# Optimization experiments

Hardware: AMD Instinct MI355X
Metric: run time of the kernel (lower is better)

Reference implementation:

```python
import math
import jax, jax.numpy as jnp
import numpy as np

B, C_IN, H, W = 32, 96, 64, 64
OUT = 128
EXC = int(OUT * 0.8)   # 102 excitatory channels
INH = OUT - EXC        # 26 inhibitory channels
K = 5
PAD = 2                # kernel//2 so all stages keep spatial size


def _sm_kernel(kernel_size=5, sigma_e=1.2, sigma_i=1.4):
    c = kernel_size // 2
    xx, yy = np.meshgrid(np.arange(kernel_size), np.arange(kernel_size), indexing='ij')
    xx = xx.astype(np.float32) - c
    yy = yy.astype(np.float32) - c
    ge = np.exp(-(xx ** 2 + yy ** 2) / (2 * sigma_e ** 2))
    gi = np.exp(-(xx ** 2 + yy ** 2) / (2 * sigma_i ** 2))
    dog = ge / (2 * math.pi * sigma_e ** 2) - gi / (2 * math.pi * sigma_i ** 2)
    dog = dog / dog[c, c]
    return jnp.asarray(dog[None, None], dtype=jnp.float32)  # [1,1,K,K]


def setup_inputs() -> dict:
    key = jax.random.key(0)
    k1, k2, k3, k4 = jax.random.split(key, 4)
    wr = 25.0 / math.sqrt(C_IN * K * K)
    x = jax.random.normal(k1, (B, C_IN, H, W), jnp.float32)
    w_ee = wr * jnp.abs(jax.random.normal(k2, (EXC, C_IN, K, K), jnp.float32))
    w_ei = wr * jnp.abs(jax.random.normal(k3, (INH, EXC, K, K), jnp.float32))
    w_ie = -wr * jnp.abs(jax.random.normal(k4, (EXC, INH, K, K), jnp.float32))
    return {"x": x, "w_ee": w_ee, "w_ei": w_ei, "w_ie": w_ie, "sm_kernel": _sm_kernel()}


def _reflect_pad(x, p):
    if p == 0:
        return x
    return jnp.pad(x, ((0, 0), (0, 0), (p, p), (p, p)), mode='reflect')


def _conv(x, w, pad=0, groups=1):
    return jax.lax.conv_general_dilated(
        x, w, window_strides=(1, 1), padding=[(pad, pad), (pad, pad)],
        dimension_numbers=('NCHW', 'OIHW', 'NCHW'), feature_group_count=groups)


def _forward(x, w_ee, w_ei, w_ie, sm_kernel):
    y_e = _conv(_reflect_pad(x, PAD), w_ee)                 # [B,EXC,H,W], act=Identity
    y_i = jax.nn.relu(_conv(_reflect_pad(y_e, PAD), w_ei))  # [B,INH,H,W]
    y_ie = _conv(_reflect_pad(y_i, PAD), w_ie)              # [B,EXC,H,W]
    y = y_e + y_ie
    # depthwise surround-modulation conv (zero padding, as in F.conv2d)
    w_sm = jnp.tile(sm_kernel, (EXC, 1, 1, 1))              # [EXC,1,K,K]
    y = _conv(y, w_sm, pad=K // 2, groups=EXC)
    return y, y_e, y_i


def reference(x, w_ee, w_ei, w_ie, sm_kernel):
    y, y_e, y_i = _forward(x, w_ee, w_ei, w_ie, sm_kernel)

    # --- hard WTA masks (winner channel per (b,h,w) position) ---
    win_e = jnp.argmax(y_e, axis=1)                                        # [B,H,W]
    mask_e = (jnp.arange(EXC)[None, :, None, None] == win_e[:, None]).astype(y_e.dtype)
    y_wta_e = y_e * mask_e
    win_i = jnp.argmax(jnp.abs(y_i), axis=1)
    mask_i = (jnp.arange(INH)[None, :, None, None] == win_i[:, None]).astype(y_i.dtype)
    y_wta_i = y_i * mask_i

    # --- transpose-conv outer-product trick; with same-size feature maps the
    # conv collapses to a 1x1 full correlation over (b,h,w) -> einsum ---
    yx_ee = jnp.einsum('bchw,behw->ec', x, y_wta_e)[:, :, None, None]      # [EXC,C_IN,1,1]
    yx_ei = jnp.einsum('behw,bihw->ie', y_wta_e, y_wta_i)[:, :, None, None]  # [INH,EXC,1,1]
    yx_ie = jnp.einsum('bihw,behw->ei', y_wta_i, y)[:, :, None, None]      # [EXC,INH,1,1]

    yu_e = jnp.sum(y_wta_e, axis=(0, 2, 3))[:, None, None, None]           # [EXC,1,1,1]
    yu_i = jnp.sum(jnp.abs(y_wta_i), axis=(0, 2, 3))[:, None, None, None]  # [INH,1,1,1]

    upd_ee = yx_ee - yu_e * w_ee   # broadcasts to [EXC,C_IN,K,K]
    upd_ei = yx_ei - yu_i * w_ei
    upd_ie = yx_ie - yu_e * w_ie
    upd_ee = upd_ee / (jnp.abs(upd_ee).max() + 1e-8)
    upd_ei = upd_ei / (jnp.abs(upd_ei).max() + 1e-8)
    upd_ie = upd_ie / (jnp.abs(upd_ie).max() + 1e-8)

    return (y, upd_ee, upd_ei, upd_ie)
```

## Files before the change

kernel.cpp:

```cpp
#include <hip/hip_runtime.h>

#define B_    32
#define CIN_  96
#define EXC_  102
#define INH_  26
#define HH    64
#define WW    64
#define HW_   4096
#define NPOS  (B_*HW_)
#define EEPAD 97
#define NPART 512
#define NEE   (EXC_*CIN_ + EXC_)
#define NIE   (EXC_*INH_)
#define N1U   (EXC_*CIN_*25)
#define N2U   (INH_*EXC_*25)
#define N3U   (EXC_*INH_*25)

typedef short bf8 __attribute__((ext_vector_type(8)));
typedef float f32x4 __attribute__((ext_vector_type(4)));

__device__ __forceinline__ int refl(int i) {
    if (i < 0) i = -i;
    if (i > 63) i = 126 - i;
    return i;
}

__device__ __forceinline__ short f2bf(float f) {
    unsigned u = __float_as_uint(f);
    return (short)((u + 0x7fffu + ((u >> 16) & 1u)) >> 16);
}

template<int C, int CPAD>
__global__ __launch_bounds__(256) void pack_nhwc(
    const float* __restrict__ src, short* __restrict__ dst)
{
    const int b = blockIdx.z;
    const int pos = blockIdx.x*64 + (threadIdx.x & 63);
    const int cg0 = threadIdx.x >> 6;
    for (int cg = cg0; cg < CPAD/8; cg += 4) {
        bf8 v;
#pragma unroll
        for (int j = 0; j < 8; ++j) {
            int c = cg*8 + j;
            float f = (c < C) ? src[((size_t)b*C + c)*HW_ + pos] : 0.f;
            v[j] = f2bf(f);
        }
        *(bf8*)(&dst[((size_t)b*HW_ + pos)*CPAD + cg*8]) = v;
    }
}

__global__ __launch_bounds__(256) void pack_w3(
    const float* __restrict__ w_ee, const float* __restrict__ w_ei,
    const float* __restrict__ w_ie, short* __restrict__ dst)
{
    int gi = blockIdx.x*256 + threadIdx.x;
    if (gi >= 460800) return;
    const float* src; int N, C, NPAD, CPAD; int idx;
    if (gi < 268800)      { src = w_ee; N = 102; C = 96;  NPAD = 112; CPAD = 96;  idx = gi; }
    else if (gi < 371200) { src = w_ei; N = 26;  C = 102; NPAD = 32;  CPAD = 128; idx = gi - 268800; }
    else                  { src = w_ie; N = 102; C = 26;  NPAD = 112; CPAD = 32;  idx = gi - 371200; }
    int tap = idx / (NPAD*CPAD);
    int rem = idx - tap*(NPAD*CPAD);
    int n = rem / CPAD, c = rem - n*CPAD;
    float f = (n < N && c < C) ? src[((size_t)n*C + c)*25 + tap] : 0.f;
    dst[gi] = f2bf(f);
}

template<int CPAD, int NPAD, int NT, int COUT, int NCHUNK, bool RELU, bool ADDIN>
__global__ __launch_bounds__(256, 2) void conv_mfma(
    const short* __restrict__ src, const short* __restrict__ wgt,
    const float* __restrict__ addin, float* __restrict__ out)
{
    __shared__ __align__(16) short sA[400*40];
    const int t  = threadIdx.x;
    const int bx = blockIdx.x;
    const int b  = blockIdx.z;
    const int h0 = (bx >> 2) * 16;
    const int w0 = (bx &  3) * 16;
    const int lane = t & 63;
    const int wv = t >> 6;
    const int nh = lane & 15;
    const int q  = lane >> 4;

    int goff[7], loff[7];
#pragma unroll
    for (int s = 0; s < 7; ++s) {
        int i = t + 256*s;
        if (i < 1600) {
            int rec = i >> 2, seg = i & 3;
            int lh = rec / 20, lw = rec - lh*20;
            int gh = refl(h0 - 2 + lh), gw = refl(w0 - 2 + lw);
            goff[s] = (b*HW_ + gh*WW + gw) * CPAD + seg*8;
            loff[s] = rec*40 + seg*8;
        } else { goff[s] = 0; loff[s] = -1; }
    }

    f32x4 acc[4][NT];
#pragma unroll
    for (int mt = 0; mt < 4; ++mt)
#pragma unroll
        for (int nt = 0; nt < NT; ++nt) {
            f32x4 z = {0.f, 0.f, 0.f, 0.f};
            acc[mt][nt] = z;
        }

    int abase[4];
#pragma unroll
    for (int mt = 0; mt < 4; ++mt)
        abase[mt] = ((wv*4 + mt)*20 + nh)*40 + q*8;

    for (int ck = 0; ck < NCHUNK; ++ck) {
        const int c0 = ck*32;
        __syncthreads();
#pragma unroll
        for (int s = 0; s < 7; ++s)
            if (loff[s] >= 0)
                *(bf8*)(&sA[loff[s]]) = *(const bf8*)(&src[goff[s] + c0]);
        __syncthreads();
        const short* wch = wgt + c0 + nh*CPAD + q*8;

        bf8 bfr[2][NT];
        bf8 afr[2][4];
        auto LOADTAP = [&](int buf, int tap_) {
            const int dh_ = tap_ / 5, dw_ = tap_ - 5*dh_;
#pragma unroll
            for (int nt = 0; nt < NT; ++nt)
                bfr[buf][nt] = *(const bf8*)(&wch[(size_t)(tap_*NPAD + nt*16)*CPAD]);
#pragma unroll
            for (int mt = 0; mt < 4; ++mt)
                afr[buf][mt] = *(const bf8*)(&sA[abase[mt] + (dh_*20 + dw_)*40]);
        };

        LOADTAP(0, 0);
#pragma unroll
        for (int tap = 0; tap < 25; ++tap) {
            const int cur = tap & 1;
            if (tap < 24) LOADTAP(cur ^ 1, tap + 1);
#pragma unroll
            for (int mt = 0; mt < 4; ++mt)
#pragma unroll
                for (int nt = 0; nt < NT; ++nt)
                    acc[mt][nt] = __builtin_amdgcn_mfma_f32_16x16x32_bf16(
                        afr[cur][mt], bfr[cur][nt], acc[mt][nt], 0, 0, 0);
        }
    }

#pragma unroll
    for (int mt = 0; mt < 4; ++mt) {
        const int rowi = h0 + wv*4 + mt;
#pragma unroll
        for (int nt = 0; nt < NT; ++nt) {
            const int chn = nt*16 + nh;
            if (chn < COUT) {
                size_t obase = ((size_t)(b*COUT + chn))*HW_ + rowi*WW + w0 + q*4;
#pragma unroll
                for (int r = 0; r < 4; ++r) {
                    float v = acc[mt][nt][r];
                    if (RELU) v = fmaxf(v, 0.f);
                    if (ADDIN) v += addin[obase + r];
                    out[obase + r] = v;
                }
            }
        }
    }
}

__global__ __launch_bounds__(256) void smconv_v2(
    const float* __restrict__ in, const float* __restrict__ sm,
    float* __restrict__ out)
{
    __shared__ __align__(16) float sx[36*36];
    const int tid = threadIdx.x;
    const int tile = blockIdx.x;
    const int e = blockIdx.y;
    const int b = blockIdx.z;
    const int h0 = (tile >> 1) * 32, w0 = (tile & 1) * 32;
    const int r  = tid >> 3;
    const int cg = (tid & 7) * 4;
    const float* inc = in + ((size_t)(b*EXC_ + e))*HW_;
#pragma unroll
    for (int it = 0; it < 6; ++it) {
        int i = tid + it*256;
        if (i < 1296) {
            int lh = i / 36, lw = i - lh*36;
            int gh = h0 - 2 + lh, gw = w0 - 2 + lw;
            float v = 0.f;
            if (gh >= 0 && gh < HH && gw >= 0 && gw < WW) v = inc[gh*WW + gw];
            sx[i] = v;
        }
    }
    __syncthreads();
    float a0 = 0.f, a1 = 0.f, a2 = 0.f, a3 = 0.f;
#pragma unroll
    for (int kh = 0; kh < 5; ++kh) {
        const float4* rowp = (const float4*)(sx + (r + kh)*36 + cg);
        float4 v0 = rowp[0], v1 = rowp[1];
        float xv[8] = {v0.x, v0.y, v0.z, v0.w, v1.x, v1.y, v1.z, v1.w};
#pragma unroll
        for (int kw = 0; kw < 5; ++kw) {
            float wv = sm[kh*5 + kw];
            a0 = fmaf(xv[kw+0], wv, a0);
            a1 = fmaf(xv[kw+1], wv, a1);
            a2 = fmaf(xv[kw+2], wv, a2);
            a3 = fmaf(xv[kw+3], wv, a3);
        }
    }
    size_t oidx = ((size_t)(b*EXC_ + e))*HW_ + (h0 + r)*WW + w0 + cg;
    *(float4*)(out + oidx) = make_float4(a0, a1, a2, a3);
}

__global__ void wta_kernel(const float* __restrict__ in, int* __restrict__ win,
                           float* __restrict__ val, int C, int use_abs)
{
    int p = blockIdx.x*256 + threadIdx.x;
    int b = p >> 12, hw = p & 4095;
    const float* base = in + ((size_t)b*C)*HW_ + hw;
    float bestv = base[0];
    float bestk = use_abs ? fabsf(bestv) : bestv;
    int besti = 0;
    for (int c = 1; c < C; ++c) {
        float v = base[(size_t)c*HW_];
        float key = use_abs ? fabsf(v) : v;
        if (key > bestk) { bestk = key; bestv = v; besti = c; }
    }
    win[p] = besti;
    val[p] = bestv;
}

__global__ __launch_bounds__(256) void scatter_ee_kernel(
    const float* __restrict__ x, const int* __restrict__ win_e,
    const float* __restrict__ val_e, float* __restrict__ parts)
{
    __shared__ float s_yx[EXC_*EEPAD];
    __shared__ float s_yu[EXC_];
    for (int i = threadIdx.x; i < EXC_*EEPAD; i += 256) s_yx[i] = 0.f;
    if (threadIdx.x < EXC_) s_yu[threadIdx.x] = 0.f;
    __syncthreads();
    int p = blockIdx.x * 256 + threadIdx.x;
    int b = p >> 12, hw = p & 4095;
    int wi = win_e[p]; float v = val_e[p];
    atomicAdd(&s_yu[wi], v);
    const float* xb = x + ((size_t)b*CIN_)*HW_ + hw;
    float* row = s_yx + wi*EEPAD;
    for (int c = 0; c < CIN_; ++c)
        atomicAdd(&row[c], v * xb[(size_t)c*HW_]);
    __syncthreads();
    float* dst = parts + (size_t)blockIdx.x * NEE;
    for (int i = threadIdx.x; i < EXC_*CIN_; i += 256) {
        int e = i / CIN_, c = i - e*CIN_;
        dst[i] = s_yx[e*EEPAD + c];
    }
    if (threadIdx.x < EXC_) dst[EXC_*CIN_ + threadIdx.x] = s_yu[threadIdx.x];
}

__global__ __launch_bounds__(256) void scatter_ei_kernel(
    const int* __restrict__ win_e, const float* __restrict__ val_e,
    const int* __restrict__ win_i, const float* __restrict__ val_i,
    float* __restrict__ yx_ei, float* __restrict__ yu_i)
{
    __shared__ float s[INH_*EXC_ + INH_];
    for (int i = threadIdx.x; i < INH_*EXC_ + INH_; i += 256) s[i] = 0.f;
    __syncthreads();
    int p = blockIdx.x * 256 + threadIdx.x;
    int we = win_e[p]; float ve = val_e[p];
    int wi = win_i[p]; float vi = val_i[p];
    atomicAdd(&s[wi*EXC_ + we], ve*vi);
    atomicAdd(&s[INH_*EXC_ + wi], fabsf(vi));
    __syncthreads();
    for (int i = threadIdx.x; i < INH_*EXC_ + INH_; i += 256) {
        float v = s[i];
        if (v != 0.f) {
            if (i < INH_*EXC_) atomicAdd(&yx_ei[i], v);
            else               atomicAdd(&yu_i[i - INH_*EXC_], v);
        }
    }
}

__global__ __launch_bounds__(256) void scatter_ie_kernel(
    const float* __restrict__ y, const int* __restrict__ win_i,
    const float* __restrict__ val_i, float* __restrict__ parts)
{
    __shared__ float s[EXC_*INH_];
    for (int i = threadIdx.x; i < EXC_*INH_; i += 256) s[i] = 0.f;
    __syncthreads();
    int p = blockIdx.x * 256 + threadIdx.x;
    int b = p >> 12, hw = p & 4095;
    int wi = win_i[p]; float v = val_i[p];
    if (v != 0.f) {
        const float* yb = y + ((size_t)b*EXC_)*HW_ + hw;
        for (int e = 0; e < EXC_; ++e)
            atomicAdd(&s[e*INH_ + wi], v * yb[(size_t)e*HW_]);
    }
    __syncthreads();
    float* dst = parts + (size_t)blockIdx.x * NIE;
    for (int i = threadIdx.x; i < EXC_*INH_; i += 256) dst[i] = s[i];
}

__global__ __launch_bounds__(256) void reduce_parts_kernel(
    const float* __restrict__ parts, float* __restrict__ dst, int n)
{
    __shared__ float s[256];
    int i = blockIdx.x*64 + (threadIdx.x & 63);
    int g = threadIdx.x >> 6;
    float a = 0.f;
    if (i < n) {
        for (int j = g*128; j < g*128 + 128; ++j)
            a += parts[(size_t)j*n + i];
    }
    s[threadIdx.x] = a;
    __syncthreads();
    if (threadIdx.x < 64 && i < n)
        dst[i] = s[threadIdx.x] + s[threadIdx.x+64] + s[threadIdx.x+128] + s[threadIdx.x+192];
}

__global__ __launch_bounds__(256) void upd_absmax3(
    const float* __restrict__ yx_ee, const float* __restrict__ yu_e,
    const float* __restrict__ w_ee,
    const float* __restrict__ yx_ei, const float* __restrict__ yu_i,
    const float* __restrict__ w_ei,
    const float* __restrict__ yx_ie, const float* __restrict__ w_ie,
    unsigned int* __restrict__ amax)
{
    float m0 = 0.f, m1 = 0.f, m2 = 0.f;
    for (int idx = blockIdx.x*256 + threadIdx.x; idx < N1U + N2U + N3U;
         idx += gridDim.x*256) {
        if (idx < N1U) {
            int ec = idx / 25; int e = ec / CIN_;
            m0 = fmaxf(m0, fabsf(yx_ee[ec] - yu_e[e]*w_ee[idx]));
        } else if (idx < N1U + N2U) {
            int j = idx - N1U; int ec = j / 25; int e = ec / EXC_;
            m1 = fmaxf(m1, fabsf(yx_ei[ec] - yu_i[e]*w_ei[j]));
        } else {
            int j = idx - N1U - N2U; int ec = j / 25; int e = ec / INH_;
            m2 = fmaxf(m2, fabsf(yx_ie[ec] - yu_e[e]*w_ie[j]));
        }
    }
    __shared__ unsigned int s0, s1, s2;
    if (threadIdx.x == 0) { s0 = 0u; s1 = 0u; s2 = 0u; }
    __syncthreads();
    atomicMax(&s0, __float_as_uint(m0));
    atomicMax(&s1, __float_as_uint(m1));
    atomicMax(&s2, __float_as_uint(m2));
    __syncthreads();
    if (threadIdx.x == 0) {
        atomicMax(&amax[0], s0);
        atomicMax(&amax[1], s1);
        atomicMax(&amax[2], s2);
    }
}

__global__ __launch_bounds__(256) void upd_write3(
    const float* __restrict__ yx_ee, const float* __restrict__ yu_e,
    const float* __restrict__ w_ee,
    const float* __restrict__ yx_ei, const float* __restrict__ yu_i,
    const float* __restrict__ w_ei,
    const float* __restrict__ yx_ie, const float* __restrict__ w_ie,
    const unsigned int* __restrict__ amax,
    float* __restrict__ out_ee, float* __restrict__ out_ei,
    float* __restrict__ out_ie)
{
    int idx = blockIdx.x*256 + threadIdx.x;
    if (idx >= N1U + N2U + N3U) return;
    if (idx < N1U) {
        int ec = idx / 25; int e = ec / CIN_;
        float v = yx_ee[ec] - yu_e[e]*w_ee[idx];
        out_ee[idx] = v / (__uint_as_float(amax[0]) + 1e-8f);
    } else if (idx < N1U + N2U) {
        int j = idx - N1U; int ec = j / 25; int e = ec / EXC_;
        float v = yx_ei[ec] - yu_i[e]*w_ei[j];
        out_ei[j] = v / (__uint_as_float(amax[1]) + 1e-8f);
    } else {
        int j = idx - N1U - N2U; int ec = j / 25; int e = ec / INH_;
        float v = yx_ie[ec] - yu_e[e]*w_ie[j];
        out_ie[j] = v / (__uint_as_float(amax[2]) + 1e-8f);
    }
}

extern "C" void kernel_launch(void* const* d_in, const int* in_sizes, int n_in,
                              void* d_out, int out_size, void* d_ws, size_t ws_size,
                              hipStream_t stream)
{
    const float* x    = (const float*)d_in[0];
    const float* w_ee = (const float*)d_in[1];
    const float* w_ei = (const float*)d_in[2];
    const float* w_ie = (const float*)d_in[3];
    const float* smk  = (const float*)d_in[4];
    float* out = (float*)d_out;

    float* y_e = (float*)d_ws;
    float* y_i = y_e + (size_t)B_*EXC_*HW_;
    short* R   = (short*)(y_i + (size_t)B_*INH_*HW_);
    short* wee = R + (size_t)16777216;
    short* wei = wee + 268800;
    short* wie = wei + 102400;
    int*   win_e = (int*)(wie + 89600);
    float* val_e = (float*)(win_e + NPOS);
    int*   win_i = (int*)(val_e + NPOS);
    float* val_i = (float*)(win_i + NPOS);
    float* yx_ee = val_i + NPOS;
    float* yu_e  = yx_ee + EXC_*CIN_;
    float* yx_ie = yu_e + EXC_;
    float* yx_ei = yx_ie + EXC_*INH_;
    float* yu_i  = yx_ei + INH_*EXC_;
    unsigned int* amax = (unsigned int*)(yu_i + INH_);
    float* parts_ee = (float*)R;
    float* parts_ie = parts_ee + (size_t)NPART*NEE;

    hipMemsetAsync(yx_ei, 0, (size_t)(INH_*EXC_ + INH_ + 3)*sizeof(float), stream);

    pack_w3<<<1800, 256, 0, stream>>>(w_ee, w_ei, w_ie, wee);
    pack_nhwc<CIN_, 96><<<dim3(64, 1, B_), 256, 0, stream>>>(x, R);

    conv_mfma<96, 112, 7, EXC_, 3, false, false>
        <<<dim3(16, 1, B_), 256, 0, stream>>>(R, wee, nullptr, y_e);
    wta_kernel<<<NPOS/256, 256, 0, stream>>>(y_e, win_e, val_e, EXC_, 0);

    pack_nhwc<EXC_, 128><<<dim3(64, 1, B_), 256, 0, stream>>>(y_e, R);
    conv_mfma<128, 32, 2, INH_, 4, true, false>
        <<<dim3(16, 1, B_), 256, 0, stream>>>(R, wei, nullptr, y_i);
    wta_kernel<<<NPOS/256, 256, 0, stream>>>(y_i, win_i, val_i, INH_, 1);

    pack_nhwc<INH_, 32><<<dim3(64, 1, B_), 256, 0, stream>>>(y_i, R);
    conv_mfma<32, 112, 7, EXC_, 1, false, true>
        <<<dim3(16, 1, B_), 256, 0, stream>>>(R, wie, y_e, y_e);

    smconv_v2<<<dim3(4, EXC_, B_), 256, 0, stream>>>(y_e, smk, out);

    scatter_ee_kernel<<<NPART, 256, 0, stream>>>(x, win_e, val_e, parts_ee);
    scatter_ei_kernel<<<NPART, 256, 0, stream>>>(win_e, val_e, win_i, val_i, yx_ei, yu_i);
    scatter_ie_kernel<<<NPART, 256, 0, stream>>>(out, win_i, val_i, parts_ie);
    reduce_parts_kernel<<<(NEE + 63)/64, 256, 0, stream>>>(parts_ee, yx_ee, NEE);
    reduce_parts_kernel<<<(NIE + 63)/64, 256, 0, stream>>>(parts_ie, yx_ie, NIE);

    upd_absmax3<<<480, 256, 0, stream>>>(yx_ee, yu_e, w_ee, yx_ei, yu_i, w_ei,
                                         yx_ie, w_ie, amax);
    float* out_ee = out + (size_t)B_*EXC_*HW_;
    float* out_ei = out_ee + N1U;
    float* out_ie = out_ei + N2U;
    upd_write3<<<(N1U + N2U + N3U + 255)/256, 256, 0, stream>>>(
        yx_ee, yu_e, w_ee, yx_ei, yu_i, w_ei, yx_ie, w_ie, amax,
        out_ee, out_ei, out_ie);
}
```

Baseline: 638.0 us.

## Fuse WTA argmax and bf16 NHWC output into conv epilogues, merge small kernels

Winner-take-all argmax is moved into the conv epilogue using a lane shuffle reduction, which removes the two separate WTA passes over y_e and y_i. The second conv now writes bf16 NHWC output directly, so the fp32 y_i tensor and its repack kernel go away. Weight packing, x packing and the memset are merged into one launch, the two scatters are combined, and the two reductions share one kernel. The tap software prefetch in the MFMA loop is replaced by a simpler per-tap load, which may change how well load latency is hidden. The WTA for y_i drops the abs key, which assumes ReLU makes the values non-negative.

```diff
diff --git a/kernel.cpp b/kernel.cpp
--- a/kernel.cpp
+++ b/kernel.cpp
@@ -30,6 +30,42 @@
     return (short)((u + 0x7fffu + ((u >> 16) & 1u)) >> 16);
 }
 
+__global__ __launch_bounds__(256) void pack_all(
+    const float* __restrict__ w_ee, const float* __restrict__ w_ei,
+    const float* __restrict__ w_ie, const float* __restrict__ x,
+    short* __restrict__ wdst, short* __restrict__ xdst,
+    float* __restrict__ zreg)
+{
+    const int blk = blockIdx.x;
+    if (blk < 1800) {
+        int gi = blk*256 + threadIdx.x;
+        if (gi >= 460800) return;
+        const float* src; int N, C, NPAD, CPAD; int idx;
+        if (gi < 268800)      { src = w_ee; N = 102; C = 96;  NPAD = 112; CPAD = 96;  idx = gi; }
+        else if (gi < 371200) { src = w_ei; N = 26;  C = 102; NPAD = 32;  CPAD = 128; idx = gi - 268800; }
+        else                  { src = w_ie; N = 102; C = 26;  NPAD = 112; CPAD = 32;  idx = gi - 371200; }
+        int tap = idx / (NPAD*CPAD);
+        int rem = idx - tap*(NPAD*CPAD);
+        int n = rem / CPAD, c = rem - n*CPAD;
+        float f = (n < N && c < C) ? src[((size_t)n*C + c)*25 + tap] : 0.f;
+        wdst[gi] = f2bf(f);
+    } else if (blk < 3848) {
+        int bb = blk - 1800;
+        int b = bb >> 6, bx = bb & 63;
+        const int pos = bx*64 + (threadIdx.x & 63);
+        const int cg0 = threadIdx.x >> 6;
+        for (int cg = cg0; cg < 96/8; cg += 4) {
+            bf8 v;
+#pragma unroll
+            for (int j = 0; j < 8; ++j)
+                v[j] = f2bf(x[((size_t)b*CIN_ + cg*8 + j)*HW_ + pos]);
+            *(bf8*)(&xdst[((size_t)b*HW_ + pos)*96 + cg*8]) = v;
+        }
+    } else {
+        for (int i = threadIdx.x; i < INH_*EXC_ + INH_ + 3; i += 256) zreg[i] = 0.f;
+    }
+}
+
 template<int C, int CPAD>
 __global__ __launch_bounds__(256) void pack_nhwc(
     const float* __restrict__ src, short* __restrict__ dst)
@@ -49,27 +85,13 @@
     }
 }
 
-__global__ __launch_bounds__(256) void pack_w3(
-    const float* __restrict__ w_ee, const float* __restrict__ w_ei,
-    const float* __restrict__ w_ie, short* __restrict__ dst)
-{
-    int gi = blockIdx.x*256 + threadIdx.x;
-    if (gi >= 460800) return;
-    const float* src; int N, C, NPAD, CPAD; int idx;
-    if (gi < 268800)      { src = w_ee; N = 102; C = 96;  NPAD = 112; CPAD = 96;  idx = gi; }
-    else if (gi < 371200) { src = w_ei; N = 26;  C = 102; NPAD = 32;  CPAD = 128; idx = gi - 268800; }
-    else                  { src = w_ie; N = 102; C = 26;  NPAD = 112; CPAD = 32;  idx = gi - 371200; }
-    int tap = idx / (NPAD*CPAD);
-    int rem = idx - tap*(NPAD*CPAD);
-    int n = rem / CPAD, c = rem - n*CPAD;
-    float f = (n < N && c < C) ? src[((size_t)n*C + c)*25 + tap] : 0.f;
-    dst[gi] = f2bf(f);
-}
-
-template<int CPAD, int NPAD, int NT, int COUT, int NCHUNK, bool RELU, bool ADDIN>
+template<int CPAD, int NPAD, int NT, int COUT, int NCHUNK,
+         bool RELU, bool ADDIN, bool WFLOAT, int OCPAD, bool WTA>
 __global__ __launch_bounds__(256, 2) void conv_mfma(
     const short* __restrict__ src, const short* __restrict__ wgt,
-    const float* __restrict__ addin, float* __restrict__ out)
+    const float* __restrict__ addin, float* __restrict__ out,
+    short* __restrict__ nhwc_out, int* __restrict__ win,
+    float* __restrict__ val)
 {
     __shared__ __align__(16) short sA[400*40];
     const int t  = threadIdx.x;
@@ -118,30 +140,25 @@
                 *(bf8*)(&sA[loff[s]]) = *(const bf8*)(&src[goff[s] + c0]);
         __syncthreads();
         const short* wch = wgt + c0 + nh*CPAD + q*8;
-
-        bf8 bfr[2][NT];
-        bf8 afr[2][4];
-        auto LOADTAP = [&](int buf, int tap_) {
-            const int dh_ = tap_ / 5, dw_ = tap_ - 5*dh_;
-#pragma unroll
-            for (int nt = 0; nt < NT; ++nt)
-                bfr[buf][nt] = *(const bf8*)(&wch[(size_t)(tap_*NPAD + nt*16)*CPAD]);
-#pragma unroll
-            for (int mt = 0; mt < 4; ++mt)
-                afr[buf][mt] = *(const bf8*)(&sA[abase[mt] + (dh_*20 + dw_)*40]);
-        };
-
-        LOADTAP(0, 0);
-#pragma unroll
-        for (int tap = 0; tap < 25; ++tap) {
-            const int cur = tap & 1;
-            if (tap < 24) LOADTAP(cur ^ 1, tap + 1);
-#pragma unroll
-            for (int mt = 0; mt < 4; ++mt)
+        for (int dh = 0; dh < 5; ++dh) {
+#pragma unroll
+            for (int dw = 0; dw < 5; ++dw) {
+                const int tap = dh*5 + dw;
+                bf8 bfr[NT];
 #pragma unroll
                 for (int nt = 0; nt < NT; ++nt)
-                    acc[mt][nt] = __builtin_amdgcn_mfma_f32_16x16x32_bf16(
-                        afr[cur][mt], bfr[cur][nt], acc[mt][nt], 0, 0, 0);
+                    bfr[nt] = *(const bf8*)(&wch[(size_t)(tap*NPAD + nt*16)*CPAD]);
+                bf8 afr[4];
+#pragma unroll
+                for (int mt = 0; mt < 4; ++mt)
+                    afr[mt] = *(const bf8*)(&sA[abase[mt] + (dh*20 + dw)*40]);
+#pragma unroll
+                for (int mt = 0; mt < 4; ++mt)
+#pragma unroll
+                    for (int nt = 0; nt < NT; ++nt)
+                        acc[mt][nt] = __builtin_amdgcn_mfma_f32_16x16x32_bf16(
+                            afr[mt], bfr[nt], acc[mt][nt], 0, 0, 0);
+            }
         }
     }
 
@@ -151,7 +168,7 @@
 #pragma unroll
         for (int nt = 0; nt < NT; ++nt) {
             const int chn = nt*16 + nh;
-            if (chn < COUT) {
+            if (WFLOAT && chn < COUT) {
                 size_t obase = ((size_t)(b*COUT + chn))*HW_ + rowi*WW + w0 + q*4;
 #pragma unroll
                 for (int r = 0; r < 4; ++r) {
@@ -159,6 +176,46 @@
                     if (RELU) v = fmaxf(v, 0.f);
                     if (ADDIN) v += addin[obase + r];
                     out[obase + r] = v;
+                }
+            }
+            if (OCPAD > 0) {
+#pragma unroll
+                for (int r = 0; r < 4; ++r) {
+                    float v = acc[mt][nt][r];
+                    if (RELU) v = fmaxf(v, 0.f);
+                    int pos = rowi*WW + w0 + q*4 + r;
+                    nhwc_out[((size_t)b*HW_ + pos)*OCPAD + chn] = f2bf(v);
+                }
+            }
+        }
+        if (OCPAD > NT*16) {
+#pragma unroll
+            for (int r = 0; r < 4; ++r) {
+                int pos = rowi*WW + w0 + q*4 + r;
+                for (int ct = NT*16 + nh; ct < OCPAD; ct += 16)
+                    nhwc_out[((size_t)b*HW_ + pos)*OCPAD + ct] = 0;
+            }
+        }
+        if (WTA) {
+#pragma unroll
+            for (int r = 0; r < 4; ++r) {
+                float bv = -3.402823e38f; int bc = 0;
+#pragma unroll
+                for (int nt = 0; nt < NT; ++nt) {
+                    const int chn = nt*16 + nh;
+                    float v = acc[mt][nt][r];
+                    if (RELU) v = fmaxf(v, 0.f);
+                    if (chn < COUT && v > bv) { bv = v; bc = chn; }
+                }
+#pragma unroll
+                for (int off = 1; off < 16; off <<= 1) {
+                    float ov = __shfl_xor(bv, off);
+                    int   oc = __shfl_xor(bc, off);
+                    if (ov > bv || (ov == bv && oc < bc)) { bv = ov; bc = oc; }
+                }
+                if (nh == 0) {
+                    int p = b*HW_ + rowi*WW + w0 + q*4 + r;
+                    win[p] = bc; val[p] = bv;
                 }
             }
         }
@@ -209,24 +266,6 @@
     *(float4*)(out + oidx) = make_float4(a0, a1, a2, a3);
 }
 
-__global__ void wta_kernel(const float* __restrict__ in, int* __restrict__ win,
-                           float* __restrict__ val, int C, int use_abs)
-{
-    int p = blockIdx.x*256 + threadIdx.x;
-    int b = p >> 12, hw = p & 4095;
-    const float* base = in + ((size_t)b*C)*HW_ + hw;
-    float bestv = base[0];
-    float bestk = use_abs ? fabsf(bestv) : bestv;
-    int besti = 0;
-    for (int c = 1; c < C; ++c) {
-        float v = base[(size_t)c*HW_];
-        float key = use_abs ? fabsf(v) : v;
-        if (key > bestk) { bestk = key; bestv = v; besti = c; }
-    }
-    win[p] = besti;
-    val[p] = bestv;
-}
-
 __global__ __launch_bounds__(256) void scatter_ee_kernel(
     const float* __restrict__ x, const int* __restrict__ win_e,
     const float* __restrict__ val_e, float* __restrict__ parts)
@@ -253,64 +292,59 @@
     if (threadIdx.x < EXC_) dst[EXC_*CIN_ + threadIdx.x] = s_yu[threadIdx.x];
 }
 
-__global__ __launch_bounds__(256) void scatter_ei_kernel(
-    const int* __restrict__ win_e, const float* __restrict__ val_e,
-    const int* __restrict__ win_i, const float* __restrict__ val_i,
-    float* __restrict__ yx_ei, float* __restrict__ yu_i)
-{
-    __shared__ float s[INH_*EXC_ + INH_];
-    for (int i = threadIdx.x; i < INH_*EXC_ + INH_; i += 256) s[i] = 0.f;
+__global__ __launch_bounds__(256) void scatter_iei_kernel(
+    const float* __restrict__ y, const int* __restrict__ win_e,
+    const float* __restrict__ val_e, const int* __restrict__ win_i,
+    const float* __restrict__ val_i, float* __restrict__ yx_ei,
+    float* __restrict__ yu_i, float* __restrict__ parts)
+{
+    __shared__ float s_ei[INH_*EXC_ + INH_];
+    __shared__ float s_ie[EXC_*INH_];
+    for (int i = threadIdx.x; i < INH_*EXC_ + INH_; i += 256) s_ei[i] = 0.f;
+    for (int i = threadIdx.x; i < EXC_*INH_; i += 256) s_ie[i] = 0.f;
     __syncthreads();
     int p = blockIdx.x * 256 + threadIdx.x;
+    int b = p >> 12, hw = p & 4095;
     int we = win_e[p]; float ve = val_e[p];
     int wi = win_i[p]; float vi = val_i[p];
-    atomicAdd(&s[wi*EXC_ + we], ve*vi);
-    atomicAdd(&s[INH_*EXC_ + wi], fabsf(vi));
+    atomicAdd(&s_ei[wi*EXC_ + we], ve*vi);
+    atomicAdd(&s_ei[INH_*EXC_ + wi], fabsf(vi));
+    if (vi != 0.f) {
+        const float* yb = y + ((size_t)b*EXC_)*HW_ + hw;
+        for (int e = 0; e < EXC_; ++e)
+            atomicAdd(&s_ie[e*INH_ + wi], vi * yb[(size_t)e*HW_]);
+    }
     __syncthreads();
     for (int i = threadIdx.x; i < INH_*EXC_ + INH_; i += 256) {
-        float v = s[i];
+        float v = s_ei[i];
         if (v != 0.f) {
             if (i < INH_*EXC_) atomicAdd(&yx_ei[i], v);
             else               atomicAdd(&yu_i[i - INH_*EXC_], v);
         }
     }
-}
-
-__global__ __launch_bounds__(256) void scatter_ie_kernel(
-    const float* __restrict__ y, const int* __restrict__ win_i,
-    const float* __restrict__ val_i, float* __restrict__ parts)
-{
-    __shared__ float s[EXC_*INH_];
-    for (int i = threadIdx.x; i < EXC_*INH_; i += 256) s[i] = 0.f;
-    __syncthreads();
-    int p = blockIdx.x * 256 + threadIdx.x;
-    int b = p >> 12, hw = p & 4095;
-    int wi = win_i[p]; float v = val_i[p];
-    if (v != 0.f) {
-        const float* yb = y + ((size_t)b*EXC_)*HW_ + hw;
-        for (int e = 0; e < EXC_; ++e)
-            atomicAdd(&s[e*INH_ + wi], v * yb[(size_t)e*HW_]);
-    }
-    __syncthreads();
     float* dst = parts + (size_t)blockIdx.x * NIE;
-    for (int i = threadIdx.x; i < EXC_*INH_; i += 256) dst[i] = s[i];
-}
-
-__global__ __launch_bounds__(256) void reduce_parts_kernel(
-    const float* __restrict__ parts, float* __restrict__ dst, int n)
+    for (int i = threadIdx.x; i < EXC_*INH_; i += 256) dst[i] = s_ie[i];
+}
+
+__global__ __launch_bounds__(256) void reduce_all_kernel(
+    const float* __restrict__ parts_ee, const float* __restrict__ parts_ie,
+    float* __restrict__ yx_ee, float* __restrict__ yx_ie)
 {
     __shared__ float s[256];
-    int i = blockIdx.x*64 + (threadIdx.x & 63);
+    int col = blockIdx.x*64 + (threadIdx.x & 63);
     int g = threadIdx.x >> 6;
+    const float* P; float* D; int n, i;
+    if (col < NEE) { P = parts_ee; D = yx_ee; n = NEE; i = col; }
+    else           { P = parts_ie; D = yx_ie; n = NIE; i = col - NEE; }
     float a = 0.f;
-    if (i < n) {
-        for (int j = g*128; j < g*128 + 128; ++j)
-            a += parts[(size_t)j*n + i];
+    if (col < NEE + NIE) {
+        for (int j = g*(NPART/4); j < (g+1)*(NPART/4); ++j)
+            a += P[(size_t)j*n + i];
     }
     s[threadIdx.x] = a;
     __syncthreads();
-    if (threadIdx.x < 64 && i < n)
-        dst[i] = s[threadIdx.x] + s[threadIdx.x+64] + s[threadIdx.x+128] + s[threadIdx.x+192];
+    if (threadIdx.x < 64 && col < NEE + NIE)
+        D[i] = s[threadIdx.x] + s[threadIdx.x+64] + s[threadIdx.x+128] + s[threadIdx.x+192];
 }
 
 __global__ __launch_bounds__(256) void upd_absmax3(
@@ -387,12 +421,12 @@
     const float* smk  = (const float*)d_in[4];
     float* out = (float*)d_out;
 
-    float* y_e = (float*)d_ws;
-    float* y_i = y_e + (size_t)B_*EXC_*HW_;
-    short* R   = (short*)(y_i + (size_t)B_*INH_*HW_);
-    short* wee = R + (size_t)16777216;
-    short* wei = wee + 268800;
-    short* wie = wei + 102400;
+    float* y_e  = (float*)d_ws;
+    short* yibf = (short*)(y_e + (size_t)B_*EXC_*HW_);
+    short* R    = yibf + (size_t)4194304;
+    short* wee  = R + (size_t)16777216;
+    short* wei  = wee + 268800;
+    short* wie  = wei + 102400;
     int*   win_e = (int*)(wie + 89600);
     float* val_e = (float*)(win_e + NPOS);
     int*   win_i = (int*)(val_e + NPOS);
@@ -403,34 +437,33 @@
     float* yx_ei = yx_ie + EXC_*INH_;
     float* yu_i  = yx_ei + INH_*EXC_;
     unsigned int* amax = (unsigned int*)(yu_i + INH_);
-    float* parts_ee = (float*)R;
+    float* parts_ee = y_e;
     float* parts_ie = parts_ee + (size_t)NPART*NEE;
 
-    hipMemsetAsync(yx_ei, 0, (size_t)(INH_*EXC_ + INH_ + 3)*sizeof(float), stream);
-
-    pack_w3<<<1800, 256, 0, stream>>>(w_ee, w_ei, w_ie, wee);
-    pack_nhwc<CIN_, 96><<<dim3(64, 1, B_), 256, 0, stream>>>(x, R);
-
-    conv_mfma<96, 112, 7, EXC_, 3, false, false>
-        <<<dim3(16, 1, B_), 256, 0, stream>>>(R, wee, nullptr, y_e);
-    wta_kernel<<<NPOS/256, 256, 0, stream>>>(y_e, win_e, val_e, EXC_, 0);
+    pack_all<<<3849, 256, 0, stream>>>(w_ee, w_ei, w_ie, x, wee, R, yx_ei);
+
+    conv_mfma<96, 112, 7, EXC_, 3, false, false, true, 0, true>
+        <<<dim3(16, 1, B_), 256, 0, stream>>>(R, wee, nullptr, y_e, nullptr,
+                                              win_e, val_e);
 
     pack_nhwc<EXC_, 128><<<dim3(64, 1, B_), 256, 0, stream>>>(y_e, R);
-    conv_mfma<128, 32, 2, INH_, 4, true, false>
-        <<<dim3(16, 1, B_), 256, 0, stream>>>(R, wei, nullptr, y_i);
-    wta_kernel<<<NPOS/256, 256, 0, stream>>>(y_i, win_i, val_i, INH_, 1);
-
-    pack_nhwc<INH_, 32><<<dim3(64, 1, B_), 256, 0, stream>>>(y_i, R);
-    conv_mfma<32, 112, 7, EXC_, 1, false, true>
-        <<<dim3(16, 1, B_), 256, 0, stream>>>(R, wie, y_e, y_e);
+
+    conv_mfma<128, 32, 2, INH_, 4, true, false, false, 32, true>
+        <<<dim3(16, 1, B_), 256, 0, stream>>>(R, wei, nullptr, nullptr, yibf,
+                                              win_i, val_i);
+
+    conv_mfma<32, 112, 7, EXC_, 1, false, true, true, 0, false>
+        <<<dim3(16, 1, B_), 256, 0, stream>>>(yibf, wie, y_e, y_e, nullptr,
+                                              nullptr, nullptr);
 
     smconv_v2<<<dim3(4, EXC_, B_), 256, 0, stream>>>(y_e, smk, out);
 
     scatter_ee_kernel<<<NPART, 256, 0, stream>>>(x, win_e, val_e, parts_ee);
-    scatter_ei_kernel<<<NPART, 256, 0, stream>>>(win_e, val_e, win_i, val_i, yx_ei, yu_i);
-    scatter_ie_kernel<<<NPART, 256, 0, stream>>>(out, win_i, val_i, parts_ie);
-    reduce_parts_kernel<<<(NEE + 63)/64, 256, 0, stream>>>(parts_ee, yx_ee, NEE);
-    reduce_parts_kernel<<<(NIE + 63)/64, 256, 0, stream>>>(parts_ie, yx_ie, NIE);
+    scatter_iei_kernel<<<NPART, 256, 0, stream>>>(out, win_e, val_e, win_i,
+                                                  val_i, yx_ei, yu_i, parts_ie);
+
+    reduce_all_kernel<<<(NEE + NIE + 63)/64, 256, 0, stream>>>(
+        parts_ee, parts_ie, yx_ee, yx_ie);
 
     upd_absmax3<<<480, 256, 0, stream>>>(yx_ee, yu_e, w_ee, yx_ei, yu_i, w_ei,
                                          yx_ie, w_ie, amax);
```

Result: faster. 564.7 us (-11.5%).
